# Kernel optimization log

Hardware: AMD Instinct MI355X
Metric: run time of the kernel (lower is better)

The kernel has to match this reference:

```python
import jax, jax.numpy as jnp
import numpy as np

B, S, D, H = 4, 2048, 1024, 16
HD = D // H
EPS = 1e-5


def setup_inputs() -> dict:
    key = jax.random.key(0)
    ks = jax.random.split(key, 12)
    scale = 1.0 / np.sqrt(D)
    inp = {
        "x": jax.random.normal(ks[0], (B, S, D), dtype=jnp.float32),
        "template_ids": jax.random.randint(ks[1], (B, S), 0, 1000, dtype=jnp.int64)
            if jax.config.jax_enable_x64 else jax.random.randint(ks[1], (B, S), 0, 1000, dtype=jnp.int32),
        "attention_mask": jnp.ones((B, S), dtype=jnp.int32),
        "Wq": jax.random.normal(ks[2], (D, D), dtype=jnp.float32) * scale,
        "bq": jnp.zeros((D,), dtype=jnp.float32),
        "Wk": jax.random.normal(ks[3], (D, D), dtype=jnp.float32) * scale,
        "bk": jnp.zeros((D,), dtype=jnp.float32),
        "Wv": jax.random.normal(ks[4], (D, D), dtype=jnp.float32) * scale,
        "bv": jnp.zeros((D,), dtype=jnp.float32),
        "Wo": jax.random.normal(ks[5], (D, D), dtype=jnp.float32) * scale,
        "bo": jnp.zeros((D,), dtype=jnp.float32),
        "gamma": jnp.ones((D,), dtype=jnp.float32),
        "beta": jnp.zeros((D,), dtype=jnp.float32),
    }
    return inp


def _split_heads(t):
    # [B,S,D] -> [B,H,S,HD]
    return t.reshape(B, S, H, HD).transpose(0, 2, 1, 3)


def reference(x, template_ids, attention_mask, Wq, bq, Wk, bk, Wv, bv, Wo, bo, gamma, beta):
    q = _split_heads(x @ Wq.T + bq)
    k = _split_heads(x @ Wk.T + bk)
    v = _split_heads(x @ Wv.T + bv)
    # [B,H,S,S]
    scores = jnp.einsum("bhqd,bhkd->bhqk", q, k) / jnp.sqrt(jnp.float32(HD))
    mask = attention_mask[:, None, None, :]  # broadcast over heads and query dim
    scores = jnp.where(mask == 0, jnp.float32(-10000.0), scores)
    attn = jax.nn.softmax(scores, axis=-1)  # dropout is identity in eval
    out = jnp.einsum("bhqk,bhkd->bhqd", attn, v)
    out = out.transpose(0, 2, 1, 3).reshape(B, S, D)
    out = out @ Wo.T + bo
    # residual + LayerNorm
    y = x + out
    mu = jnp.mean(y, axis=-1, keepdims=True)
    var = jnp.var(y, axis=-1, keepdims=True)
    return (y - mu) * jax.lax.rsqrt(var + EPS) * gamma + beta
```

## Files before the change

### kernel.cpp

```cpp
#include <hip/hip_runtime.h>

typedef unsigned short u16;
typedef unsigned int u32;
typedef __attribute__((ext_vector_type(8))) short bf16x8;
typedef __attribute__((ext_vector_type(4))) float f32x4;

#define NB 4
#define SS 2048
#define DD 1024
#define NH 16
#define HD 64
#define MM (NB*SS)

struct __align__(16) Pack16 { unsigned int w0, w1, w2, w3; };
union PU { Pack16 p; u16 s[8]; };

__device__ __forceinline__ float b2f(u16 u) {
    union { unsigned int i; float f; } v; v.i = ((unsigned int)u) << 16; return v.f;
}
__device__ __forceinline__ u16 f2b(float f) {
    union { unsigned int i; float f; } v; v.f = f;
    return (u16)((v.i + 0x7FFFu + ((v.i >> 16) & 1u)) >> 16);
}
__device__ __forceinline__ float rdS(const void* p, size_t i, int mode) {
    return mode ? ((const float*)p)[i] : b2f(((const u16*)p)[i]);
}
__device__ __forceinline__ float ex2(float x) { return __builtin_amdgcn_exp2f(x); }
__device__ __forceinline__ u32 cvtpk(float lo, float hi) {
    u32 r;
    asm("v_cvt_pk_bf16_f32 %0, %1, %2" : "=v"(r) : "v"(lo), "v"(hi));
    return r;
}

__device__ __forceinline__ void cp16(const u16* g, u16* l) {
    __builtin_amdgcn_global_load_lds(
        (const __attribute__((address_space(1))) void*)g,
        (__attribute__((address_space(3))) void*)l, 16, 0, 0);
}

__device__ __forceinline__ void pl32swap(u32& a, u32& b) {
    asm volatile("v_permlane32_swap_b32 %0, %1" : "+v"(a), "+v"(b));
}
__device__ __forceinline__ void pl16swap(u32& a, u32& b) {
    asm volatile("v_permlane16_swap_b32 %0, %1" : "+v"(a), "+v"(b));
}

#define QSC 0.1803368801111204f
#define GX ((size_t)MM * DD / 8)
#define GW ((size_t)DD * DD / 8)
#define GTOT (GX + 4 * GW + 512)

__global__ __launch_bounds__(256) void convert_kernel(
    const void* __restrict__ x,
    const void* __restrict__ Wq, const void* __restrict__ Wk,
    const void* __restrict__ Wv, const void* __restrict__ Wo,
    const void* __restrict__ bq, const void* __restrict__ bk,
    const void* __restrict__ bv, const void* __restrict__ bo,
    u16* __restrict__ xb, u16* __restrict__ Wc, u16* __restrict__ Wob,
    u16* __restrict__ bcat, const u32* __restrict__ gamma_w)
{
    const int mode = (gamma_w[0] == 0x3F800000u) ? 1 : 0;
    size_t g = (size_t)blockIdx.x * 256 + threadIdx.x;
    const void* src; u16* dst; size_t off; float sc = 1.0f;
    if (g < GX)               { src = x;  dst = xb;              off = g * 8; }
    else if (g < GX + GW)     { src = Wq; dst = Wc;              off = (g - GX) * 8; sc = QSC; }
    else if (g < GX + 2 * GW) { src = Wk; dst = Wc + (size_t)DD * DD;     off = (g - GX - GW) * 8; }
    else if (g < GX + 3 * GW) { src = Wv; dst = Wc + (size_t)2 * DD * DD; off = (g - GX - 2 * GW) * 8; }
    else if (g < GX + 4 * GW) { src = Wo; dst = Wob;             off = (g - GX - 3 * GW) * 8; }
    else {
        size_t gg = g - (GX + 4 * GW);
        int which = (int)(gg >> 7); off = (gg & 127) * 8;
        src = (which == 0) ? bq : (which == 1) ? bk : (which == 2) ? bv : bo;
        dst = bcat + which * DD;
        if (which == 0) sc = QSC;
    }
    PU o;
    if (mode) {
        const float* s = (const float*)src + off;
        float4 a = ((const float4*)s)[0];
        float4 b = ((const float4*)s)[1];
        o.s[0] = f2b(a.x * sc); o.s[1] = f2b(a.y * sc);
        o.s[2] = f2b(a.z * sc); o.s[3] = f2b(a.w * sc);
        o.s[4] = f2b(b.x * sc); o.s[5] = f2b(b.y * sc);
        o.s[6] = f2b(b.z * sc); o.s[7] = f2b(b.w * sc);
    } else {
        PU in; in.p = *(const Pack16*)((const u16*)src + off);
#pragma unroll
        for (int j = 0; j < 8; j++) o.s[j] = f2b(b2f(in.s[j]) * sc);
    }
    *(Pack16*)(dst + off) = o.p;
}

__global__ __launch_bounds__(256) void gemm_qkv(
    const u16* __restrict__ xb, const u16* __restrict__ Wc, const u16* __restrict__ bcat,
    u16* __restrict__ Q, u16* __restrict__ K, u16* __restrict__ V)
{
    __shared__ __align__(16) u16 sh[2 * 128 * 64];
    u16* As = sh;
    u16* Bs = sh + 128 * 64;

    const int tid  = threadIdx.x;
    const int wv   = tid >> 6;
    const int lane = tid & 63;
    const int wy = wv >> 1, wx = wv & 1;
    const int l15 = lane & 15, quad = lane >> 4;
    const int m0 = blockIdx.x * 128, n0 = blockIdx.y * 128;
    const int srow = lane >> 3;
    const int sw   = ((lane & 7) ^ srow) * 8;
    const int key  = l15 & 7;

    f32x4 acc[4][4];
#pragma unroll
    for (int i = 0; i < 4; i++)
#pragma unroll
        for (int j = 0; j < 4; j++) acc[i][j] = (f32x4){0.f, 0.f, 0.f, 0.f};

    for (int k0 = 0; k0 < DD; k0 += 64) {
#pragma unroll
        for (int c = 0; c < 4; c++) {
            cp16(&xb[(size_t)(m0 + wv * 32 + c * 8 + srow) * DD + k0 + sw],
                 &As[wv * 2048 + c * 512]);
            cp16(&Wc[(size_t)(n0 + wv * 32 + c * 8 + srow) * DD + k0 + sw],
                 &Bs[wv * 2048 + c * 512]);
        }
        __syncthreads();
#pragma unroll
        for (int ks = 0; ks < 2; ks++) {
            bf16x8 a[4], bb[4];
#pragma unroll
            for (int mt = 0; mt < 4; mt++)
                a[mt] = *(const bf16x8*)&As[(wy * 64 + mt * 16 + l15) * 64 +
                                            (((ks << 2) + quad) ^ key) * 8];
#pragma unroll
            for (int nt = 0; nt < 4; nt++)
                bb[nt] = *(const bf16x8*)&Bs[(wx * 64 + nt * 16 + l15) * 64 +
                                             (((ks << 2) + quad) ^ key) * 8];
#pragma unroll
            for (int mt = 0; mt < 4; mt++)
#pragma unroll
                for (int nt = 0; nt < 4; nt++)
                    acc[mt][nt] = __builtin_amdgcn_mfma_f32_16x16x32_bf16(
                        a[mt], bb[nt], acc[mt][nt], 0, 0, 0);
        }
        __syncthreads();
    }

    const int z = n0 >> 10;
    if (z != 2) {
        u16* out = (z == 0) ? Q : K;
#pragma unroll
        for (int nt = 0; nt < 4; nt++) {
            int n_g = n0 + wx * 64 + nt * 16 + l15;
            float bv_ = b2f(bcat[n_g]);
            int nn = n_g & 1023;
            int h = nn >> 6, hd = nn & 63;
#pragma unroll
            for (int mt = 0; mt < 4; mt++) {
#pragma unroll
                for (int r = 0; r < 4; r++) {
                    int m_g = m0 + wy * 64 + mt * 16 + quad * 4 + r;
                    int b = m_g >> 11, s = m_g & (SS - 1);
                    out[(((size_t)(b * NH + h) * SS) + s) * HD + hd] =
                        f2b(acc[mt][nt][r] + bv_);
                }
            }
        }
    } else {
        const int bb_ = m0 >> 11, sbase = m0 & (SS - 1);
#pragma unroll
        for (int ph = 0; ph < 2; ph++) {
            if (wx == ph) {
#pragma unroll
                for (int nt = 0; nt < 4; nt++) {
                    int n_loc = nt * 16 + l15;
                    float bv_ = b2f(bcat[n0 + ph * 64 + n_loc]);
#pragma unroll
                    for (int mt = 0; mt < 4; mt++) {
                        int m = wy * 64 + mt * 16 + quad * 4;
                        uint2 wr;
                        wr.x = (u32)f2b(acc[mt][nt][0] + bv_) |
                               ((u32)f2b(acc[mt][nt][1] + bv_) << 16);
                        wr.y = (u32)f2b(acc[mt][nt][2] + bv_) |
                               ((u32)f2b(acc[mt][nt][3] + bv_) << 16);
                        *(uint2*)&sh[n_loc * 136 + m] = wr;
                    }
                }
            }
            __syncthreads();
            {
                int row = tid >> 2;
                int sg  = tid & 3;
                int n_g = n0 + ph * 64 + row;
                int nn = n_g & 1023;
                int h = nn >> 6, hd = nn & 63;
                u16* dst = &V[(((size_t)(bb_ * NH + h)) * HD + hd) * SS + sbase];
#pragma unroll
                for (int j = 0; j < 4; j++) {
                    int mloc = sg * 32 + j * 8;
                    *(Pack16*)&dst[mloc] = *(const Pack16*)&sh[row * 136 + mloc];
                }
            }
            __syncthreads();
        }
    }
}

__global__ __launch_bounds__(256, 4) void attn_kernel(
    const u16* __restrict__ Q, const u16* __restrict__ K, const u16* __restrict__ V,
    const int* __restrict__ mask, u16* __restrict__ O)
{
    const int bh = blockIdx.y;
    const int b = bh >> 4, h = bh & 15;
    const int q0 = blockIdx.x * 128;
    const u16* Qp  = Q + (size_t)bh * SS * HD;
    const u16* Kp  = K + (size_t)bh * SS * HD;
    const u16* Vtg = V + (size_t)bh * HD * SS;
    const int* mk = mask + b * SS;

    __shared__ __align__(16) u16 Kl[2 * 64 * 64];
    __shared__ __align__(16) u16 Vt[2 * 64 * 64];
    __shared__ int s_anymask;

    const int tid  = threadIdx.x;
    const int w    = tid >> 6;
    const int lane = tid & 63;
    const int l15 = lane & 15, quad = lane >> 4;
    const int srow = lane >> 3;
    const int sw   = ((lane & 7) ^ srow) * 8;
    const int key  = l15 & 7;

    if (tid == 0) s_anymask = 0;
    __syncthreads();
    {
        int local = 0;
#pragma unroll
        for (int i = 0; i < 2; i++) {
            int4 m4 = ((const int4*)mk)[i * 256 + tid];
            if ((m4.x == 0) | (m4.y == 0) | (m4.z == 0) | (m4.w == 0)) local = 1;
        }
        if (local) s_anymask = 1;
    }
    __syncthreads();
    const bool anymask = (s_anymask != 0);

    bf16x8 qf[2][2];
#pragma unroll
    for (int qt = 0; qt < 2; qt++)
#pragma unroll
        for (int ks = 0; ks < 2; ks++)
            qf[qt][ks] = *(const bf16x8*)&Qp[(size_t)(q0 + w * 32 + qt * 16 + l15) * HD +
                                             ks * 32 + quad * 8];

    bf16x8 onesf;
#pragma unroll
    for (int i = 0; i < 8; i++) onesf[i] = (short)0x3F80;

    f32x4 oacc[2][4];
#pragma unroll
    for (int i = 0; i < 2; i++)
#pragma unroll
        for (int j = 0; j < 4; j++) oacc[i][j] = (f32x4){0.f, 0.f, 0.f, 0.f};
    f32x4 sumacc[2];
#pragma unroll
    for (int i = 0; i < 2; i++) sumacc[i] = (f32x4){0.f, 0.f, 0.f, 0.f};

#pragma unroll
    for (int c = 0; c < 2; c++) {
        cp16(&Kp[(size_t)(w * 16 + c * 8 + srow) * HD + sw], &Kl[w * 1024 + c * 512]);
        cp16(&Vtg[(size_t)(w * 16 + c * 8 + srow) * SS + sw], &Vt[w * 1024 + c * 512]);
    }

    for (int it = 0; it < SS / 64; it++) {
        const int kv0 = it * 64;
        const int p = it & 1;
        __syncthreads();

        if (it + 1 < SS / 64) {
            const int kn = kv0 + 64;
#pragma unroll
            for (int c = 0; c < 2; c++) {
                cp16(&Kp[(size_t)(kn + w * 16 + c * 8 + srow) * HD + sw],
                     &Kl[(p ^ 1) * 4096 + w * 1024 + c * 512]);
                cp16(&Vtg[(size_t)(w * 16 + c * 8 + srow) * SS + kn + sw],
                     &Vt[(p ^ 1) * 4096 + w * 1024 + c * 512]);
            }
        }

        f32x4 sacc[4][2];
#pragma unroll
        for (int i = 0; i < 4; i++)
#pragma unroll
            for (int j = 0; j < 2; j++) sacc[i][j] = (f32x4){0.f, 0.f, 0.f, 0.f};
#pragma unroll
        for (int ks = 0; ks < 2; ks++) {
            bf16x8 kf[4];
#pragma unroll
            for (int kvt = 0; kvt < 4; kvt++)
                kf[kvt] = *(const bf16x8*)&Kl[p * 4096 + (kvt * 16 + l15) * 64 +
                                              (((ks << 2) + quad) ^ key) * 8];
            __builtin_amdgcn_s_setprio(1);
#pragma unroll
            for (int kvt = 0; kvt < 4; kvt++)
#pragma unroll
                for (int qt = 0; qt < 2; qt++)
                    sacc[kvt][qt] = __builtin_amdgcn_mfma_f32_16x16x32_bf16(
                        kf[kvt], qf[qt][ks], sacc[kvt][qt], 0, 0, 0);
            __builtin_amdgcn_s_setprio(0);
        }

        union { bf16x8 v; u32 d[4]; } paf[2][2];
#pragma unroll
        for (int qt = 0; qt < 2; qt++) {
            u32 pk[4][2];
#pragma unroll
            for (int kvt = 0; kvt < 4; kvt++) {
                f32x4 vv = sacc[kvt][qt];
                if (anymask) {
#pragma unroll
                    for (int r = 0; r < 4; r++) {
                        int kv = kv0 + kvt * 16 + quad * 4 + r;
                        if (mk[kv] == 0) vv[r] = -20000.0f;
                    }
                }
                pk[kvt][0] = cvtpk(ex2(vv[0]), ex2(vv[1]));
                pk[kvt][1] = cvtpk(ex2(vv[2]), ex2(vv[3]));
            }
#pragma unroll
            for (int ks2 = 0; ks2 < 2; ks2++) {
#pragma unroll
                for (int c = 0; c < 2; c++) {
                    u32 x0 = pk[ks2 * 2 + 0][c];
                    u32 x1 = pk[ks2 * 2 + 1][c];
                    pl32swap(x0, x1);
                    pl16swap(x0, x1);
                    paf[qt][ks2].d[c]     = x0;
                    paf[qt][ks2].d[2 + c] = x1;
                }
            }
        }

#pragma unroll
        for (int ks2 = 0; ks2 < 2; ks2++) {
            bf16x8 vf[4];
#pragma unroll
            for (int nt = 0; nt < 4; nt++)
                vf[nt] = *(const bf16x8*)&Vt[p * 4096 + (nt * 16 + l15) * 64 +
                                             (((ks2 << 2) + quad) ^ key) * 8];
            __builtin_amdgcn_s_setprio(1);
#pragma unroll
            for (int qt = 0; qt < 2; qt++) {
#pragma unroll
                for (int nt = 0; nt < 4; nt++)
                    oacc[qt][nt] = __builtin_amdgcn_mfma_f32_16x16x32_bf16(
                        paf[qt][ks2].v, vf[nt], oacc[qt][nt], 0, 0, 0);
                sumacc[qt] = __builtin_amdgcn_mfma_f32_16x16x32_bf16(
                    paf[qt][ks2].v, onesf, sumacc[qt], 0, 0, 0);
            }
            __builtin_amdgcn_s_setprio(0);
        }
    }

#pragma unroll
    for (int qt = 0; qt < 2; qt++) {
#pragma unroll
        for (int r = 0; r < 4; r++) {
            float inv = 1.0f / sumacc[qt][r];
            int row = q0 + w * 32 + qt * 16 + quad * 4 + r;
            size_t base = ((size_t)(b * SS + row)) * DD + h * HD;
#pragma unroll
            for (int nt = 0; nt < 4; nt++)
                O[base + nt * 16 + l15] = f2b(oacc[qt][nt][r] * inv);
        }
    }
}

__global__ __launch_bounds__(256) void gemm_oproj(
    const u16* __restrict__ A, const u16* __restrict__ Wob, const u16* __restrict__ bcat,
    u16* __restrict__ Y)
{
    __shared__ __align__(16) u16 As[128 * 64];
    __shared__ __align__(16) u16 Bs[128 * 64];

    const int tid  = threadIdx.x;
    const int wv   = tid >> 6;
    const int lane = tid & 63;
    const int wy = wv >> 1, wx = wv & 1;
    const int l15 = lane & 15, quad = lane >> 4;
    const int m0 = blockIdx.x * 128, n0 = blockIdx.y * 128;
    const int srow = lane >> 3;
    const int sw   = ((lane & 7) ^ srow) * 8;
    const int key  = l15 & 7;

    f32x4 acc[4][4];
#pragma unroll
    for (int i = 0; i < 4; i++)
#pragma unroll
        for (int j = 0; j < 4; j++) acc[i][j] = (f32x4){0.f, 0.f, 0.f, 0.f};

    for (int k0 = 0; k0 < DD; k0 += 64) {
#pragma unroll
        for (int c = 0; c < 4; c++) {
            cp16(&A[(size_t)(m0 + wv * 32 + c * 8 + srow) * DD + k0 + sw],
                 &As[wv * 2048 + c * 512]);
            cp16(&Wob[(size_t)(n0 + wv * 32 + c * 8 + srow) * DD + k0 + sw],
                 &Bs[wv * 2048 + c * 512]);
        }
        __syncthreads();
#pragma unroll
        for (int ks = 0; ks < 2; ks++) {
            bf16x8 a[4], bb[4];
#pragma unroll
            for (int mt = 0; mt < 4; mt++)
                a[mt] = *(const bf16x8*)&As[(wy * 64 + mt * 16 + l15) * 64 +
                                            (((ks << 2) + quad) ^ key) * 8];
#pragma unroll
            for (int nt = 0; nt < 4; nt++)
                bb[nt] = *(const bf16x8*)&Bs[(wx * 64 + nt * 16 + l15) * 64 +
                                             (((ks << 2) + quad) ^ key) * 8];
#pragma unroll
            for (int mt = 0; mt < 4; mt++)
#pragma unroll
                for (int nt = 0; nt < 4; nt++)
                    acc[mt][nt] = __builtin_amdgcn_mfma_f32_16x16x32_bf16(
                        a[mt], bb[nt], acc[mt][nt], 0, 0, 0);
        }
        __syncthreads();
    }

#pragma unroll
    for (int nt = 0; nt < 4; nt++) {
        int n_g = n0 + wx * 64 + nt * 16 + l15;
        float bv_ = b2f(bcat[3 * DD + n_g]);
#pragma unroll
        for (int mt = 0; mt < 4; mt++) {
#pragma unroll
            for (int r = 0; r < 4; r++) {
                int m_g = m0 + wy * 64 + mt * 16 + quad * 4 + r;
                Y[(size_t)m_g * DD + n_g] = f2b(acc[mt][nt][r] + bv_);
            }
        }
    }
}

__global__ __launch_bounds__(256) void ln_kernel(
    const u16* __restrict__ Yp, const void* __restrict__ x,
    const void* __restrict__ gamma, const void* __restrict__ beta,
    void* __restrict__ out)
{
    const int mode = (((const u32*)gamma)[0] == 0x3F800000u) ? 1 : 0;
    const int w    = threadIdx.x >> 6;
    const int lane = threadIdx.x & 63;
    const int row  = blockIdx.x * 4 + w;
    const u16* y = Yp + (size_t)row * DD;

    float vals[16];
    float s = 0.f, sq = 0.f;
#pragma unroll
    for (int i = 0; i < 2; i++) {
        PU d; d.p = *(const Pack16*)&y[i * 512 + lane * 8];
        if (mode) {
            const float* xp = (const float*)x + (size_t)row * DD + i * 512 + lane * 8;
            float4 xa = ((const float4*)xp)[0];
            float4 xb2 = ((const float4*)xp)[1];
            float xr[8] = {xa.x, xa.y, xa.z, xa.w, xb2.x, xb2.y, xb2.z, xb2.w};
#pragma unroll
            for (int j = 0; j < 8; j++) {
                float f = b2f(d.s[j]) + xr[j];
                vals[i * 8 + j] = f;
                s += f; sq += f * f;
            }
        } else {
            const u16* xp = (const u16*)x + (size_t)row * DD + i * 512 + lane * 8;
            PU xd; xd.p = *(const Pack16*)xp;
#pragma unroll
            for (int j = 0; j < 8; j++) {
                float f = b2f(d.s[j]) + b2f(xd.s[j]);
                vals[i * 8 + j] = f;
                s += f; sq += f * f;
            }
        }
    }
#pragma unroll
    for (int off = 1; off < 64; off <<= 1) {
        s  += __shfl_xor(s, off);
        sq += __shfl_xor(sq, off);
    }
    float mu  = s * (1.0f / 1024.0f);
    float var = sq * (1.0f / 1024.0f) - mu * mu;
    float rs  = rsqrtf(var + 1e-5f);

#pragma unroll
    for (int i = 0; i < 2; i++) {
        float r8[8];
#pragma unroll
        for (int j = 0; j < 8; j++) {
            int col = i * 512 + lane * 8 + j;
            r8[j] = (vals[i * 8 + j] - mu) * rs * rdS(gamma, col, mode) + rdS(beta, col, mode);
        }
        if (mode) {
            float* of = (float*)out + (size_t)row * DD + i * 512 + lane * 8;
            ((float4*)of)[0] = make_float4(r8[0], r8[1], r8[2], r8[3]);
            ((float4*)of)[1] = make_float4(r8[4], r8[5], r8[6], r8[7]);
        } else {
            PU ob;
#pragma unroll
            for (int j = 0; j < 8; j++) ob.s[j] = f2b(r8[j]);
            *(Pack16*)((u16*)out + (size_t)row * DD + i * 512 + lane * 8) = ob.p;
        }
    }
}

extern "C" void kernel_launch(void* const* d_in, const int* in_sizes, int n_in,
                              void* d_out, int out_size, void* d_ws, size_t ws_size,
                              hipStream_t stream)
{
    const void* x     = d_in[0];
    const int* mask   = (const int*)d_in[2];
    const void* Wq    = d_in[3];
    const void* bq    = d_in[4];
    const void* Wk    = d_in[5];
    const void* bk    = d_in[6];
    const void* Wv    = d_in[7];
    const void* bv    = d_in[8];
    const void* Wo    = d_in[9];
    const void* bo    = d_in[10];
    const void* gamma = d_in[11];
    const void* beta  = d_in[12];

    const size_t n = (size_t)MM * DD;
    u16* xb   = (u16*)((char*)d_ws + 256);
    u16* Wc   = xb + n;
    u16* Wob  = Wc + (size_t)3 * DD * DD;
    u16* bcat = Wob + (size_t)DD * DD;
    u16* Qb   = bcat + 4096;
    u16* Kb   = Qb + n;
    u16* Vb   = Kb + n;
    u16* Ab   = Vb + n;
    u16* Yb   = xb;

    convert_kernel<<<(unsigned)(GTOT / 256), 256, 0, stream>>>(
        x, Wq, Wk, Wv, Wo, bq, bk, bv, bo, xb, Wc, Wob, bcat, (const u32*)gamma);
    gemm_qkv<<<dim3(MM / 128, 3 * DD / 128), 256, 0, stream>>>(xb, Wc, bcat, Qb, Kb, Vb);
    attn_kernel<<<dim3(SS / 128, NB * NH), 256, 0, stream>>>(Qb, Kb, Vb, mask, Ab);
    gemm_oproj<<<dim3(MM / 128, DD / 128), 256, 0, stream>>>(Ab, Wob, bcat, Yb);
    ln_kernel<<<MM / 4, 256, 0, stream>>>(Yb, x, gamma, beta, d_out);
}
```

Before: 324.6 us.

## Split output-projection GEMM over K into two partials summed in LayerNorm

The output-projection GEMM grid gains a z dimension of 2, and each block reduces over half of the K dimension. The two bf16 partial results are written into the now-free Q and K buffers, and the LayerNorm kernel sums them with the residual. This doubles the number of blocks in a GEMM that previously had only 512 tiles, which should fill the GPU better. In exchange it adds an extra partial-result write and read, plus an extra bf16 rounding step. The attention P·V stage is also reordered to interleave the exp/pack of each kv half with its MFMA, which should lower register pressure.

```diff
diff --git a/kernel.cpp b/kernel.cpp
--- a/kernel.cpp
+++ b/kernel.cpp
@@ -308,53 +308,49 @@
             __builtin_amdgcn_s_setprio(0);
         }
 
-        union { bf16x8 v; u32 d[4]; } paf[2][2];
-#pragma unroll
-        for (int qt = 0; qt < 2; qt++) {
-            u32 pk[4][2];
-#pragma unroll
-            for (int kvt = 0; kvt < 4; kvt++) {
-                f32x4 vv = sacc[kvt][qt];
-                if (anymask) {
-#pragma unroll
-                    for (int r = 0; r < 4; r++) {
-                        int kv = kv0 + kvt * 16 + quad * 4 + r;
-                        if (mk[kv] == 0) vv[r] = -20000.0f;
+#pragma unroll
+        for (int g = 0; g < 2; g++) {
+            union { bf16x8 v; u32 d[4]; } pafq[2];
+#pragma unroll
+            for (int qt = 0; qt < 2; qt++) {
+                u32 pk[2][2];
+#pragma unroll
+                for (int kk = 0; kk < 2; kk++) {
+                    const int kvt = 2 * g + kk;
+                    f32x4 vv = sacc[kvt][qt];
+                    if (anymask) {
+#pragma unroll
+                        for (int r = 0; r < 4; r++) {
+                            int kv = kv0 + kvt * 16 + quad * 4 + r;
+                            if (mk[kv] == 0) vv[r] = -20000.0f;
+                        }
                     }
+                    pk[kk][0] = cvtpk(ex2(vv[0]), ex2(vv[1]));
+                    pk[kk][1] = cvtpk(ex2(vv[2]), ex2(vv[3]));
                 }
-                pk[kvt][0] = cvtpk(ex2(vv[0]), ex2(vv[1]));
-                pk[kvt][1] = cvtpk(ex2(vv[2]), ex2(vv[3]));
-            }
-#pragma unroll
-            for (int ks2 = 0; ks2 < 2; ks2++) {
 #pragma unroll
                 for (int c = 0; c < 2; c++) {
-                    u32 x0 = pk[ks2 * 2 + 0][c];
-                    u32 x1 = pk[ks2 * 2 + 1][c];
+                    u32 x0 = pk[0][c], x1 = pk[1][c];
                     pl32swap(x0, x1);
                     pl16swap(x0, x1);
-                    paf[qt][ks2].d[c]     = x0;
-                    paf[qt][ks2].d[2 + c] = x1;
+                    pafq[qt].d[c]     = x0;
+                    pafq[qt].d[2 + c] = x1;
                 }
             }
-        }
-
-#pragma unroll
-        for (int ks2 = 0; ks2 < 2; ks2++) {
             bf16x8 vf[4];
 #pragma unroll
             for (int nt = 0; nt < 4; nt++)
                 vf[nt] = *(const bf16x8*)&Vt[p * 4096 + (nt * 16 + l15) * 64 +
-                                             (((ks2 << 2) + quad) ^ key) * 8];
+                                             (((g << 2) + quad) ^ key) * 8];
             __builtin_amdgcn_s_setprio(1);
 #pragma unroll
             for (int qt = 0; qt < 2; qt++) {
 #pragma unroll
                 for (int nt = 0; nt < 4; nt++)
                     oacc[qt][nt] = __builtin_amdgcn_mfma_f32_16x16x32_bf16(
-                        paf[qt][ks2].v, vf[nt], oacc[qt][nt], 0, 0, 0);
+                        pafq[qt].v, vf[nt], oacc[qt][nt], 0, 0, 0);
                 sumacc[qt] = __builtin_amdgcn_mfma_f32_16x16x32_bf16(
-                    paf[qt][ks2].v, onesf, sumacc[qt], 0, 0, 0);
+                    pafq[qt].v, onesf, sumacc[qt], 0, 0, 0);
             }
             __builtin_amdgcn_s_setprio(0);
         }
@@ -376,7 +372,7 @@
 
 __global__ __launch_bounds__(256) void gemm_oproj(
     const u16* __restrict__ A, const u16* __restrict__ Wob, const u16* __restrict__ bcat,
-    u16* __restrict__ Y)
+    u16* __restrict__ Y0, u16* __restrict__ Y1)
 {
     __shared__ __align__(16) u16 As[128 * 64];
     __shared__ __align__(16) u16 Bs[128 * 64];
@@ -387,6 +383,8 @@
     const int wy = wv >> 1, wx = wv & 1;
     const int l15 = lane & 15, quad = lane >> 4;
     const int m0 = blockIdx.x * 128, n0 = blockIdx.y * 128;
+    const int kz = blockIdx.z;
+    const int kbase = kz * (DD / 2);
     const int srow = lane >> 3;
     const int sw   = ((lane & 7) ^ srow) * 8;
     const int key  = l15 & 7;
@@ -397,12 +395,12 @@
 #pragma unroll
         for (int j = 0; j < 4; j++) acc[i][j] = (f32x4){0.f, 0.f, 0.f, 0.f};
 
-    for (int k0 = 0; k0 < DD; k0 += 64) {
+    for (int k0 = 0; k0 < DD / 2; k0 += 64) {
 #pragma unroll
         for (int c = 0; c < 4; c++) {
-            cp16(&A[(size_t)(m0 + wv * 32 + c * 8 + srow) * DD + k0 + sw],
+            cp16(&A[(size_t)(m0 + wv * 32 + c * 8 + srow) * DD + kbase + k0 + sw],
                  &As[wv * 2048 + c * 512]);
-            cp16(&Wob[(size_t)(n0 + wv * 32 + c * 8 + srow) * DD + k0 + sw],
+            cp16(&Wob[(size_t)(n0 + wv * 32 + c * 8 + srow) * DD + kbase + k0 + sw],
                  &Bs[wv * 2048 + c * 512]);
         }
         __syncthreads();
@@ -427,10 +425,11 @@
         __syncthreads();
     }
 
+    u16* Y = kz ? Y1 : Y0;
 #pragma unroll
     for (int nt = 0; nt < 4; nt++) {
         int n_g = n0 + wx * 64 + nt * 16 + l15;
-        float bv_ = b2f(bcat[3 * DD + n_g]);
+        float bv_ = kz ? 0.f : b2f(bcat[3 * DD + n_g]);
 #pragma unroll
         for (int mt = 0; mt < 4; mt++) {
 #pragma unroll
@@ -443,7 +442,8 @@
 }
 
 __global__ __launch_bounds__(256) void ln_kernel(
-    const u16* __restrict__ Yp, const void* __restrict__ x,
+    const u16* __restrict__ Y0p, const u16* __restrict__ Y1p,
+    const void* __restrict__ x,
     const void* __restrict__ gamma, const void* __restrict__ beta,
     void* __restrict__ out)
 {
@@ -451,13 +451,15 @@
     const int w    = threadIdx.x >> 6;
     const int lane = threadIdx.x & 63;
     const int row  = blockIdx.x * 4 + w;
-    const u16* y = Yp + (size_t)row * DD;
+    const u16* y0 = Y0p + (size_t)row * DD;
+    const u16* y1 = Y1p + (size_t)row * DD;
 
     float vals[16];
     float s = 0.f, sq = 0.f;
 #pragma unroll
     for (int i = 0; i < 2; i++) {
-        PU d; d.p = *(const Pack16*)&y[i * 512 + lane * 8];
+        PU d0; d0.p = *(const Pack16*)&y0[i * 512 + lane * 8];
+        PU d1; d1.p = *(const Pack16*)&y1[i * 512 + lane * 8];
         if (mode) {
             const float* xp = (const float*)x + (size_t)row * DD + i * 512 + lane * 8;
             float4 xa = ((const float4*)xp)[0];
@@ -465,7 +467,7 @@
             float xr[8] = {xa.x, xa.y, xa.z, xa.w, xb2.x, xb2.y, xb2.z, xb2.w};
 #pragma unroll
             for (int j = 0; j < 8; j++) {
-                float f = b2f(d.s[j]) + xr[j];
+                float f = b2f(d0.s[j]) + b2f(d1.s[j]) + xr[j];
                 vals[i * 8 + j] = f;
                 s += f; sq += f * f;
             }
@@ -474,7 +476,7 @@
             PU xd; xd.p = *(const Pack16*)xp;
 #pragma unroll
             for (int j = 0; j < 8; j++) {
-                float f = b2f(d.s[j]) + b2f(xd.s[j]);
+                float f = b2f(d0.s[j]) + b2f(d1.s[j]) + b2f(xd.s[j]);
                 vals[i * 8 + j] = f;
                 s += f; sq += f * f;
             }
@@ -536,12 +538,11 @@
     u16* Kb   = Qb + n;
     u16* Vb   = Kb + n;
     u16* Ab   = Vb + n;
-    u16* Yb   = xb;
 
     convert_kernel<<<(unsigned)(GTOT / 256), 256, 0, stream>>>(
         x, Wq, Wk, Wv, Wo, bq, bk, bv, bo, xb, Wc, Wob, bcat, (const u32*)gamma);
     gemm_qkv<<<dim3(MM / 128, 3 * DD / 128), 256, 0, stream>>>(xb, Wc, bcat, Qb, Kb, Vb);
     attn_kernel<<<dim3(SS / 128, NB * NH), 256, 0, stream>>>(Qb, Kb, Vb, mask, Ab);
-    gemm_oproj<<<dim3(MM / 128, DD / 128), 256, 0, stream>>>(Ab, Wob, bcat, Yb);
-    ln_kernel<<<MM / 4, 256, 0, stream>>>(Yb, x, gamma, beta, d_out);
-}
+    gemm_oproj<<<dim3(MM / 128, DD / 128, 2), 256, 0, stream>>>(Ab, Wob, bcat, Qb, Kb);
+    ln_kernel<<<MM / 4, 256, 0, stream>>>(Qb, Kb, x, gamma, beta, d_out);
+}
```

New measurement: 326.4 us. About the same (+0.5%).
